# Optimization experiments

Measured on AMD Instinct MI355X. Metric: run time of the kernel, lower is better.

The kernel has to match this reference:

```python
import math
import jax, jax.numpy as jnp
import numpy as np

V, D, H, L, F, S, B = 32000, 768, 12, 6, 3072, 2048, 4
DK = D // H


def setup_inputs() -> dict:
    key = jax.random.key(0)
    ks = jax.random.split(key, 16)
    sc = 0.02
    n = jax.random.normal
    inp = {
        "input_ids": jax.random.randint(ks[0], (B, S), 0, V, dtype=jnp.int64)
        if jax.config.jax_enable_x64 else jax.random.randint(ks[0], (B, S), 0, V, dtype=jnp.int32),
        "emb": n(ks[1], (V, D), jnp.float32) * sc,
        "Wq": n(ks[2], (L, D, D), jnp.float32) * sc, "bq": jnp.zeros((L, D), jnp.float32),
        "Wk": n(ks[3], (L, D, D), jnp.float32) * sc, "bk": jnp.zeros((L, D), jnp.float32),
        "Wv": n(ks[4], (L, D, D), jnp.float32) * sc, "bv": jnp.zeros((L, D), jnp.float32),
        "Wo": n(ks[5], (L, D, D), jnp.float32) * sc, "bo": jnp.zeros((L, D), jnp.float32),
        "W1": n(ks[6], (L, D, F), jnp.float32) * sc, "b1": jnp.zeros((L, F), jnp.float32),
        "W2": n(ks[7], (L, F, D), jnp.float32) * sc, "b2": jnp.zeros((L, D), jnp.float32),
        "gamma": jnp.ones((L, D), jnp.float32), "beta": jnp.zeros((L, D), jnp.float32),
    }
    return inp


def _pos_encoding(seq_len, d):
    pos = jnp.arange(seq_len, dtype=jnp.float32)[:, None]                  # [S,1]
    div = jnp.exp(jnp.arange(0, d, 2, dtype=jnp.float32) * (-math.log(10000.0) / d))
    ang = pos * div                                                        # [S,D/2]
    return jnp.stack([jnp.sin(ang), jnp.cos(ang)], axis=-1).reshape(seq_len, d)


def _layernorm(x, g, b, eps=1e-5):
    mu = x.mean(-1, keepdims=True)
    var = ((x - mu) ** 2).mean(-1, keepdims=True)
    return (x - mu) * jax.lax.rsqrt(var + eps) * g + b


def _forward(input_ids, emb, Wq, bq, Wk, bk, Wv, bv, Wo, bo, W1, b1, W2, b2, gamma, beta):
    mask = (input_ids != 1)[:, None, None, :]                              # [B,1,1,S]
    x = emb[input_ids] + _pos_encoding(input_ids.shape[1], emb.shape[1])   # [B,S,D]

    def layer(x, p):
        wq, bq_, wk, bk_, wv, bv_, wo, bo_, w1, b1_, w2, b2_, g, bt = p
        def heads(h):  # [B,S,D] -> [B,H,S,DK]
            return h.reshape(B, S, H, DK).transpose(0, 2, 1, 3)
        q = heads(x @ wq + bq_)
        k = heads(x @ wk + bk_)
        v = heads(x @ wv + bv_)
        scores = jnp.einsum("bhqd,bhkd->bhqk", q, k) / math.sqrt(DK)
        scores = jnp.where(mask, scores, -1e9)
        attn = jax.nn.softmax(scores, axis=-1)
        o = jnp.einsum("bhqk,bhkd->bhqd", attn, v)
        o = o.transpose(0, 2, 1, 3).reshape(B, S, D) @ wo + bo_
        x1 = _layernorm(x + o, g, bt)
        ff = jax.nn.relu(x1 @ w1 + b1_) @ w2 + b2_
        return _layernorm(x1 + ff, g, bt), None  # same norm params reused (as in source)

    x, _ = jax.lax.scan(layer, x, (Wq, bq, Wk, bk, Wv, bv, Wo, bo, W1, b1, W2, b2, gamma, beta))
    return x.mean(axis=1)                                                  # [B,D]


def reference(input_ids, emb, Wq, bq, Wk, bk, Wv, bv, Wo, bo, W1, b1, W2, b2, gamma, beta):
    return _forward(input_ids, emb, Wq, bq, Wk, bk, Wv, bv, Wo, bo, W1, b1, W2, b2, gamma, beta)
```

## Files before the change

kernel.cpp:

```cpp
#include <hip/hip_runtime.h>
#include <hip/hip_bf16.h>
#include <math.h>

typedef unsigned short u16;
typedef unsigned long long u64;
using bf16x8 = __attribute__((ext_vector_type(8))) short;
using f32x4  = __attribute__((ext_vector_type(4))) float;

static constexpr int kD = 768;
static constexpr int kH = 12;
static constexpr int kL = 6;
static constexpr int kF = 3072;
static constexpr int kS = 2048;
static constexpr int kB = 4;
static constexpr int kQW = 2304;
static constexpr int kNT = kB * kS;

static constexpr float kQScale = 0.18033688011112043f;

__device__ __forceinline__ u16 f2bf(float f) {
    return __bfloat16_as_ushort(__float2bfloat16(f));
}
__device__ __forceinline__ float b2f(u16 u) {
    return __uint_as_float((unsigned)u << 16);
}
__device__ __forceinline__ unsigned cvtpk(float a, float b) {
    unsigned d;
    asm volatile("v_cvt_pk_bf16_f32 %0, %1, %2" : "=v"(d) : "v"(a), "v"(b));
    return d;
}
__device__ __forceinline__ float exp2fast(float x) {
#if __has_builtin(__builtin_amdgcn_exp2f)
    return __builtin_amdgcn_exp2f(x);
#else
    return __expf(x * 0.6931471805599453f);
#endif
}

__device__ __forceinline__ void gload16(const void* g, void* l) {
    auto gp = reinterpret_cast<const __attribute__((address_space(1))) unsigned int*>(
        reinterpret_cast<uintptr_t>(g));
    auto lp = reinterpret_cast<__attribute__((address_space(3))) unsigned int*>(
        reinterpret_cast<uintptr_t>(l));
    __builtin_amdgcn_global_load_lds(gp, lp, 16, 0, 0);
}

__global__ __launch_bounds__(256) void embed_pe(
    const int* __restrict__ ids, const float* __restrict__ emb,
    u16* __restrict__ xbf)
{
    const int t = blockIdx.x;
    const int s = t & (kS - 1);
    const int id = ids[t];
#pragma unroll
    for (int j = 0; j < 3; ++j) {
        const int d = threadIdx.x + (j << 8);
        const float i2 = (float)((d >> 1) << 1);
        const float dv = __expf(i2 * (-9.210340371976184f / 768.f));
        const float ang = (float)s * dv;
        const float pe = (d & 1) ? cosf(ang) : sinf(ang);
        xbf[(size_t)t * kD + d] = f2bf(emb[(size_t)id * kD + d] + pe);
    }
}

__global__ __launch_bounds__(256) void embed_pe_f32(
    const int* __restrict__ ids, const float* __restrict__ emb,
    float* __restrict__ x)
{
    const int t = blockIdx.x;
    const int s = t & (kS - 1);
    const int id = ids[t];
#pragma unroll
    for (int j = 0; j < 3; ++j) {
        const int d = threadIdx.x + (j << 8);
        const float i2 = (float)((d >> 1) << 1);
        const float dv = __expf(i2 * (-9.210340371976184f / 768.f));
        const float ang = (float)s * dv;
        const float pe = (d & 1) ? cosf(ang) : sinf(ang);
        x[(size_t)t * kD + d] = emb[(size_t)id * kD + d] + pe;
    }
}

__global__ __launch_bounds__(64) void mk_maskbits(const int* __restrict__ ids,
                                                  u64* __restrict__ mbits)
{
    const int w = blockIdx.x;
    const int lane = threadIdx.x;
    const u64 m = __ballot(ids[(size_t)w * 64 + lane] != 1);
    if (lane == 0) mbits[w] = m;
}

__global__ __launch_bounds__(256) void bias_build(
    const float* __restrict__ bq, const float* __restrict__ bk,
    const float* __restrict__ bv, const float* __restrict__ bo,
    const float* __restrict__ b1, const float* __restrict__ b2,
    float* __restrict__ ba)
{
    const int i = blockIdx.x * 256 + threadIdx.x;
    if (i >= 6 * 6912) return;
    const int l = i / 6912, p = i % 6912;
    float v;
    if      (p < 768)  v = bq[l * 768 + p] * kQScale;
    else if (p < 1536) v = bk[l * 768 + p - 768];
    else if (p < 2304) v = bv[l * 768 + p - 1536];
    else if (p < 3072) v = bo[l * 768 + p - 2304];
    else if (p < 6144) v = b1[(size_t)l * 3072 + p - 3072];
    else               v = b2[l * 768 + p - 6144];
    ba[i] = v;
}

static constexpr size_t OFF_WO = (size_t)2304 * 768;
static constexpr size_t OFF_W1 = OFF_WO + (size_t)768 * 768;
static constexpr size_t OFF_W2 = OFF_W1 + (size_t)3072 * 768;
static constexpr size_t WARENA_E = OFF_W2 + (size_t)768 * 3072;

__global__ __launch_bounds__(256) void cvt_all(
    const float* __restrict__ Wq, const float* __restrict__ Wk,
    const float* __restrict__ Wv, const float* __restrict__ Wo,
    const float* __restrict__ W1, const float* __restrict__ W2,
    u16* __restrict__ wa)
{
    __shared__ float T[64][68];
    const int t = blockIdx.x;
    const float* S; u16* Dp; int Nsrc, Kdst, srow0, scol0; float sc = 1.f;
    if (t < 432) {
        const int ni = t % 36, ki = t / 36;
        const int ng = ni * 64;
        const int sel = ng / 768;
        scol0 = ng % 768; srow0 = ki * 64;
        S = (sel == 0) ? Wq : (sel == 1) ? Wk : Wv;
        if (sel == 0) sc = kQScale;
        Nsrc = 768; Kdst = 768;
        Dp = wa + (size_t)ng * 768 + srow0;
    } else if (t < 576) {
        const int tt = t - 432; const int ni = tt % 12, ki = tt / 12;
        scol0 = ni * 64; srow0 = ki * 64;
        S = Wo; Nsrc = 768; Kdst = 768;
        Dp = wa + OFF_WO + (size_t)(ni * 64) * 768 + srow0;
    } else if (t < 1152) {
        const int tt = t - 576; const int ni = tt % 48, ki = tt / 48;
        scol0 = ni * 64; srow0 = ki * 64;
        S = W1; Nsrc = 3072; Kdst = 768;
        Dp = wa + OFF_W1 + (size_t)(ni * 64) * 768 + srow0;
    } else {
        const int tt = t - 1152; const int ni = tt % 12, ki = tt / 12;
        scol0 = ni * 64; srow0 = ki * 64;
        S = W2; Nsrc = 768; Kdst = 3072;
        Dp = wa + OFF_W2 + (size_t)(ni * 64) * 3072 + srow0;
    }
    const int tid = threadIdx.x;
#pragma unroll
    for (int i = 0; i < 4; ++i) {
        const int idx = tid + (i << 8);
        const int kr = idx >> 4;
        const int nc = (idx & 15) << 2;
        const float4 v = *(const float4*)(S + (size_t)(srow0 + kr) * Nsrc + scol0 + nc);
        T[kr][nc] = v.x; T[kr][nc + 1] = v.y; T[kr][nc + 2] = v.z; T[kr][nc + 3] = v.w;
    }
    __syncthreads();
#pragma unroll
    for (int i = 0; i < 4; ++i) {
        const int idx = tid + (i << 8);
        const int nr = idx >> 4;
        const int kc = (idx & 15) << 2;
        ushort4 o;
        o.x = f2bf(T[kc][nr] * sc);     o.y = f2bf(T[kc + 1][nr] * sc);
        o.z = f2bf(T[kc + 2][nr] * sc); o.w = f2bf(T[kc + 3][nr] * sc);
        *(ushort4*)(Dp + (size_t)nr * Kdst + kc) = o;
    }
}

__global__ __launch_bounds__(256, 2) void gemm256b(
    const u16* __restrict__ A, const u16* __restrict__ Bt,
    const float* __restrict__ bias, void* __restrict__ Cv,
    u16* __restrict__ vTp, int M, int N, int K, int mode)
{
    __shared__ u16 As[3][4096];
    __shared__ u16 Bs[3][8192];
    const int tid = threadIdx.x;
    const int l = tid & 63;
    const int lo = l & 15, hi = l >> 4;
    const int wc = tid >> 6;

    int brow = blockIdx.x, bcol = blockIdx.y;
    const int gx = gridDim.x;
    if ((gx & 7) == 0) {
        const int id = blockIdx.y * gx + blockIdx.x;
        const int xcd = id & 7, idx = id >> 3;
        const int rpx = gx >> 3;
        brow = xcd * rpx + (idx % rpx);
        bcol = idx / rpx;
    }
    const size_t row0 = (size_t)brow * 128;
    const size_t col0 = (size_t)bcol * 256;

    const int ca0 = tid, ca1 = tid + 256;
    const int ra0 = ca0 >> 2, ga0 = (ca0 & 3) ^ ((ra0 >> 1) & 3);
    const int ra1 = ca1 >> 2, ga1 = (ca1 & 3) ^ ((ra1 >> 1) & 3);
    const u16* aP0 = A + (row0 + ra0) * K + ga0 * 8;
    const u16* aP1 = A + (row0 + ra1) * K + ga1 * 8;
    const u16* bP[4];
#pragma unroll
    for (int q = 0; q < 4; ++q) {
        const int c = tid + (q << 8);
        const int r = c >> 2, g = (c & 3) ^ ((r >> 1) & 3);
        bP[q] = Bt + (col0 + r) * K + g * 8;
    }

    f32x4 acc[8][4];
#pragma unroll
    for (int i = 0; i < 8; ++i)
#pragma unroll
        for (int j = 0; j < 4; ++j)
#pragma unroll
            for (int r = 0; r < 4; ++r) acc[i][j][r] = 0.f;

    int aoff[8], boff[4];
#pragma unroll
    for (int i = 0; i < 8; ++i) {
        const int ra = i * 16 + lo;
        aoff[i] = ra * 32 + ((hi ^ ((ra >> 1) & 3)) << 3);
    }
#pragma unroll
    for (int j = 0; j < 4; ++j) {
        const int rb = wc * 64 + j * 16 + lo;
        boff[j] = rb * 32 + ((hi ^ ((rb >> 1) & 3)) << 3);
    }

    const int NT = K >> 5;
#pragma unroll
    for (int t = 0; t < 2; ++t) {
        const int k0 = t << 5;
        gload16(aP0 + k0, As[t] + ca0 * 8);
        gload16(aP1 + k0, As[t] + ca1 * 8);
#pragma unroll
        for (int q = 0; q < 4; ++q)
            gload16(bP[q] + k0, Bs[t] + (tid + (q << 8)) * 8);
    }

    int cur = 0;
    for (int t = 0; t < NT; ++t) {
        if (t + 1 < NT) {
            asm volatile("s_waitcnt vmcnt(6)" ::: "memory");
        } else {
            asm volatile("s_waitcnt vmcnt(0)" ::: "memory");
        }
        __builtin_amdgcn_s_barrier();
        if (t + 2 < NT) {
            const int k0 = (t + 2) << 5;
            const int nb = (cur + 2 >= 3) ? cur - 1 : cur + 2;
            gload16(aP0 + k0, As[nb] + ca0 * 8);
            gload16(aP1 + k0, As[nb] + ca1 * 8);
#pragma unroll
            for (int q = 0; q < 4; ++q)
                gload16(bP[q] + k0, Bs[nb] + (tid + (q << 8)) * 8);
        }
        bf16x8 af[8], bfr[4];
#pragma unroll
        for (int i = 0; i < 8; ++i) af[i]  = *(const bf16x8*)&As[cur][aoff[i]];
#pragma unroll
        for (int j = 0; j < 4; ++j) bfr[j] = *(const bf16x8*)&Bs[cur][boff[j]];
        __builtin_amdgcn_s_setprio(1);
#pragma unroll
        for (int i = 0; i < 8; ++i)
#pragma unroll
            for (int j = 0; j < 4; ++j)
                acc[i][j] = __builtin_amdgcn_mfma_f32_16x16x32_bf16(
                    af[i], bfr[j], acc[i][j], 0, 0, 0);
        __builtin_amdgcn_s_setprio(0);
        cur = (cur + 1 == 3) ? 0 : cur + 1;
    }

    const bool vmode = (mode == 3) && (col0 >= 1536);
    if (vmode) {
#pragma unroll
        for (int i = 0; i < 8; ++i) {
            const size_t rbase = row0 + i * 16 + hi * 4;
            const size_t tb = (rbase >> 6) * 64;
            const int k0 = (int)(rbase & 63);
            const int pos = (((k0 >> 2) & 3) << 3) + (((k0 >> 4) & 1) << 2)
                          + ((k0 >> 5) << 5);
#pragma unroll
            for (int j = 0; j < 4; ++j) {
                const size_t c = col0 + wc * 64 + j * 16 + lo;
                const float bs = bias[c];
                const size_t d = c - 1536;
                ushort4 o;
                o.x = f2bf(acc[i][j][0] + bs);
                o.y = f2bf(acc[i][j][1] + bs);
                o.z = f2bf(acc[i][j][2] + bs);
                o.w = f2bf(acc[i][j][3] + bs);
                *(ushort4*)(vTp + d * (size_t)M + tb + pos) = o;
            }
        }
        return;
    }

#pragma unroll
    for (int i = 0; i < 8; ++i) {
        const size_t rbase = row0 + i * 16 + hi * 4;
#pragma unroll
        for (int j = 0; j < 4; ++j) {
            const size_t c = col0 + wc * 64 + j * 16 + lo;
            const float bs = bias[c];
#pragma unroll
            for (int r = 0; r < 4; ++r) {
                float v = acc[i][j][r] + bs;
                if (mode == 2) v = fmaxf(v, 0.f);
                ((u16*)Cv)[(rbase + r) * (size_t)N + c] = f2bf(v);
            }
        }
    }
}

__global__ __launch_bounds__(256) void gemm_bf16(
    const u16* __restrict__ A, const u16* __restrict__ Bt,
    const float* __restrict__ bias, void* __restrict__ Cv,
    u16* __restrict__ vTp, int M, int N, int K, int mode)
{
    __shared__ u16 As[3][4096];
    __shared__ u16 Bs[3][4096];
    const int tid = threadIdx.x;
    const int l = tid & 63;
    const int lo = l & 15, hi = l >> 4;
    const int w = tid >> 6, wr = w >> 1, wc = w & 1;

    int brow = blockIdx.x, bcol = blockIdx.y;
    const int gx = gridDim.x;
    if ((gx & 7) == 0) {
        const int id = blockIdx.y * gx + blockIdx.x;
        const int xcd = id & 7, idx = id >> 3;
        const int rpx = gx >> 3;
        brow = xcd * rpx + (idx % rpx);
        bcol = idx / rpx;
    }
    const size_t row0 = (size_t)brow * 128;
    const size_t col0 = (size_t)bcol * 128;

    const int c0 = tid, c1 = tid + 256;
    const int r0 = c0 >> 2, g0 = (c0 & 3) ^ ((r0 >> 1) & 3);
    const int r1 = c1 >> 2, g1 = (c1 & 3) ^ ((r1 >> 1) & 3);
    const u16* a0 = A  + (row0 + r0) * K + g0 * 8;
    const u16* a1 = A  + (row0 + r1) * K + g1 * 8;
    const u16* b0 = Bt + (col0 + r0) * K + g0 * 8;
    const u16* b1 = Bt + (col0 + r1) * K + g1 * 8;

    f32x4 acc[4][4];
#pragma unroll
    for (int i = 0; i < 4; ++i)
#pragma unroll
        for (int j = 0; j < 4; ++j)
#pragma unroll
            for (int r = 0; r < 4; ++r) acc[i][j][r] = 0.f;

    int aoff[4], boff[4];
#pragma unroll
    for (int i = 0; i < 4; ++i) {
        const int ra = wr * 64 + i * 16 + lo;
        aoff[i] = ra * 32 + ((hi ^ ((ra >> 1) & 3)) << 3);
        const int rb = wc * 64 + i * 16 + lo;
        boff[i] = rb * 32 + ((hi ^ ((rb >> 1) & 3)) << 3);
    }

    const int NT = K >> 5;
#pragma unroll
    for (int t = 0; t < 2; ++t) {
        const int k0 = t << 5;
        gload16(a0 + k0, As[t] + c0 * 8);
        gload16(a1 + k0, As[t] + c1 * 8);
        gload16(b0 + k0, Bs[t] + c0 * 8);
        gload16(b1 + k0, Bs[t] + c1 * 8);
    }

    int cur = 0;
    for (int t = 0; t < NT; ++t) {
        if (t + 1 < NT) {
            asm volatile("s_waitcnt vmcnt(4)" ::: "memory");
        } else {
            asm volatile("s_waitcnt vmcnt(0)" ::: "memory");
        }
        __builtin_amdgcn_s_barrier();
        if (t + 2 < NT) {
            const int k0 = (t + 2) << 5;
            const int nb = (cur + 2 >= 3) ? cur - 1 : cur + 2;
            gload16(a0 + k0, As[nb] + c0 * 8);
            gload16(a1 + k0, As[nb] + c1 * 8);
            gload16(b0 + k0, Bs[nb] + c0 * 8);
            gload16(b1 + k0, Bs[nb] + c1 * 8);
        }
        bf16x8 af[4], bfr[4];
#pragma unroll
        for (int i = 0; i < 4; ++i) af[i]  = *(const bf16x8*)&As[cur][aoff[i]];
#pragma unroll
        for (int j = 0; j < 4; ++j) bfr[j] = *(const bf16x8*)&Bs[cur][boff[j]];
        __builtin_amdgcn_s_setprio(1);
#pragma unroll
        for (int i = 0; i < 4; ++i)
#pragma unroll
            for (int j = 0; j < 4; ++j)
                acc[i][j] = __builtin_amdgcn_mfma_f32_16x16x32_bf16(
                    af[i], bfr[j], acc[i][j], 0, 0, 0);
        __builtin_amdgcn_s_setprio(0);
        cur = (cur + 1 == 3) ? 0 : cur + 1;
    }

#pragma unroll
    for (int i = 0; i < 4; ++i) {
        const size_t rbase = row0 + wr * 64 + i * 16 + hi * 4;
#pragma unroll
        for (int j = 0; j < 4; ++j) {
            const size_t c = col0 + wc * 64 + j * 16 + lo;
            const float bs = bias[c];
#pragma unroll
            for (int r = 0; r < 4; ++r) {
                float v = acc[i][j][r] + bs;
                if (mode == 2) v = fmaxf(v, 0.f);
                ((u16*)Cv)[(rbase + r) * (size_t)N + c] = f2bf(v);
            }
        }
    }
}

__global__ __launch_bounds__(512) void attn_mfma(
    const u16* __restrict__ QKV, const u16* __restrict__ vT,
    const u64* __restrict__ mbits, u16* __restrict__ O)
{
    __shared__ u16 Ks[3][4096];
    __shared__ u16 Vs[3][4096];

    const int tid = threadIdx.x, l = tid & 63, w = tid >> 6;
    const int lo = l & 15, hi = l >> 4;

    const int flat = blockIdx.x + 16 * (blockIdx.y + 12 * blockIdx.z);
    const int nf = (flat & 7) * 96 + (flat >> 3);
    const int qi = nf & 15;
    const int h  = (nf >> 4) % 12;
    const int b  = nf / 192;
    const int q0 = qi << 7;

    bf16x8 qf0, qf1;
    {
        const u16* qp = QKV + ((size_t)(b * kS + q0 + w * 16 + lo)) * kQW
                            + h * 64 + hi * 8;
        qf0 = *(const bf16x8*)qp;
        qf1 = *(const bf16x8*)(qp + 32);
    }

    const int rw = tid >> 3, sx = tid & 7, E = sx ^ (rw & 7);
    const u16* Kbase = QKV + (size_t)(b * kS) * kQW + 768 + h * 64;
    const u16* Vbase = vT + (size_t)(h * 64) * kNT + b * kS;

    f32x4 accO[4];
#pragma unroll
    for (int n = 0; n < 4; ++n)
#pragma unroll
        for (int r = 0; r < 4; ++r) accO[n][r] = 0.f;
    float m = -3.0e38f, lsum = 0.f;

    const int ksw = (lo & 7) << 3;
    constexpr int NTt = kS / 64;

#pragma unroll
    for (int t = 0; t < 2; ++t) {
        const size_t kof = (size_t)(t << 6) * kQW;
        const size_t vof = (size_t)(t << 6);
        gload16(Kbase + kof + (size_t)rw * kQW + E * 8, Ks[t] + tid * 8);
        gload16(Vbase + (size_t)rw * kNT + vof + E * 8, Vs[t] + tid * 8);
    }

    int cur = 0;
    for (int kt = 0; kt < NTt; ++kt) {
        if (kt + 1 < NTt) {
            asm volatile("s_waitcnt vmcnt(2)" ::: "memory");
        } else {
            asm volatile("s_waitcnt vmcnt(0)" ::: "memory");
        }
        __syncthreads();

        if (kt + 2 < NTt) {
            const size_t kof = (size_t)((kt + 2) << 6) * kQW;
            const size_t vof = (size_t)((kt + 2) << 6);
            const int nb = (cur + 2 >= 3) ? cur - 1 : cur + 2;
            gload16(Kbase + kof + (size_t)rw * kQW + E * 8, Ks[nb] + tid * 8);
            gload16(Vbase + (size_t)rw * kNT + vof + E * 8, Vs[nb] + tid * 8);
        }

        f32x4 st[4];
        __builtin_amdgcn_s_setprio(1);
#pragma unroll
        for (int j = 0; j < 4; ++j) {
#pragma unroll
            for (int r = 0; r < 4; ++r) st[j][r] = 0.f;
            const int kb2 = (j * 16 + lo) * 64;
            const bf16x8 k0 = *(const bf16x8*)&Ks[cur][kb2 + ((hi * 8)      ^ ksw)];
            const bf16x8 k1 = *(const bf16x8*)&Ks[cur][kb2 + ((hi * 8 + 32) ^ ksw)];
            st[j] = __builtin_amdgcn_mfma_f32_16x16x32_bf16(k0, qf0, st[j], 0, 0, 0);
            st[j] = __builtin_amdgcn_mfma_f32_16x16x32_bf16(k1, qf1, st[j], 0, 0, 0);
        }
        __builtin_amdgcn_s_setprio(0);

        float rmax = st[0][0];
#pragma unroll
        for (int j = 0; j < 4; ++j)
#pragma unroll
            for (int r = 0; r < 4; ++r) rmax = fmaxf(rmax, st[j][r]);
        rmax = fmaxf(rmax, __shfl_xor(rmax, 16));
        rmax = fmaxf(rmax, __shfl_xor(rmax, 32));

        const bool skip = __all(rmax <= m + 11.0f);
        if (!skip) {
            const float mn = fmaxf(m, rmax);
            const float corr = exp2fast(m - mn);
            m = mn;
            lsum *= corr;
            float c2[4];
#pragma unroll
            for (int r = 0; r < 4; ++r) c2[r] = __shfl(corr, hi * 4 + r);
#pragma unroll
            for (int n = 0; n < 4; ++n)
#pragma unroll
                for (int r = 0; r < 4; ++r) accO[n][r] *= c2[r];
        }

#pragma unroll
        for (int j = 0; j < 4; ++j)
#pragma unroll
            for (int r = 0; r < 4; ++r) st[j][r] = exp2fast(st[j][r] - m);

        const u64 mb = mbits[b * 32 + kt];
        if (mb != ~0ull) {
#pragma unroll
            for (int j = 0; j < 4; ++j)
#pragma unroll
                for (int r = 0; r < 4; ++r)
                    if (!((mb >> (j * 16 + hi * 4 + r)) & 1)) st[j][r] = 0.f;
        }

        float ts = 0.f;
#pragma unroll
        for (int j = 0; j < 4; ++j)
#pragma unroll
            for (int r = 0; r < 4; ++r) ts += st[j][r];
        ts += __shfl_xor(ts, 16);
        ts += __shfl_xor(ts, 32);
        lsum += ts;

        union PU { unsigned u[4]; bf16x8 v; } p0, p1;
        p0.u[0] = cvtpk(st[0][0], st[0][1]); p0.u[1] = cvtpk(st[0][2], st[0][3]);
        p0.u[2] = cvtpk(st[1][0], st[1][1]); p0.u[3] = cvtpk(st[1][2], st[1][3]);
        p1.u[0] = cvtpk(st[2][0], st[2][1]); p1.u[1] = cvtpk(st[2][2], st[2][3]);
        p1.u[2] = cvtpk(st[3][0], st[3][1]); p1.u[3] = cvtpk(st[3][2], st[3][3]);

        __builtin_amdgcn_s_setprio(1);
#pragma unroll
        for (int n = 0; n < 4; ++n) {
            const int vb2 = (n * 16 + lo) * 64;
            const bf16x8 v0 = *(const bf16x8*)&Vs[cur][vb2 + ((hi * 8)      ^ ksw)];
            const bf16x8 v1 = *(const bf16x8*)&Vs[cur][vb2 + ((hi * 8 + 32) ^ ksw)];
            accO[n] = __builtin_amdgcn_mfma_f32_16x16x32_bf16(p0.v, v0, accO[n], 0, 0, 0);
            accO[n] = __builtin_amdgcn_mfma_f32_16x16x32_bf16(p1.v, v1, accO[n], 0, 0, 0);
        }
        __builtin_amdgcn_s_setprio(0);
        cur = (cur + 1 == 3) ? 0 : cur + 1;
    }

    float linv[4];
#pragma unroll
    for (int r = 0; r < 4; ++r) linv[r] = 1.f / __shfl(lsum, hi * 4 + r);
#pragma unroll
    for (int n = 0; n < 4; ++n)
#pragma unroll
        for (int r = 0; r < 4; ++r)
            O[((size_t)(b * kS + q0 + w * 16 + hi * 4 + r)) * kD
              + h * 64 + n * 16 + lo] = f2bf(accO[n][r] * linv[r]);
}

__global__ __launch_bounds__(256) void add_ln_bf(
    const u16* __restrict__ a, const u16* __restrict__ r,
    const float* __restrict__ g, const float* __restrict__ bt,
    u16* __restrict__ out)
{
    const int lane = threadIdx.x & 63;
    const size_t row = (size_t)blockIdx.x * 4 + (threadIdx.x >> 6);
    const ushort4* a4 = (const ushort4*)(a + row * kD);
    const ushort4* r4 = (const ushort4*)(r + row * kD);
    float v[3][4];
    float s = 0.f;
#pragma unroll
    for (int j = 0; j < 3; ++j) {
        const ushort4 av = a4[j * 64 + lane];
        const ushort4 rv = r4[j * 64 + lane];
        v[j][0] = b2f(av.x) + b2f(rv.x);
        v[j][1] = b2f(av.y) + b2f(rv.y);
        v[j][2] = b2f(av.z) + b2f(rv.z);
        v[j][3] = b2f(av.w) + b2f(rv.w);
        s += v[j][0] + v[j][1] + v[j][2] + v[j][3];
    }
#pragma unroll
    for (int off = 32; off; off >>= 1) s += __shfl_xor(s, off);
    const float mu = s * (1.f / 768.f);
    float vs = 0.f;
#pragma unroll
    for (int j = 0; j < 3; ++j)
#pragma unroll
        for (int e = 0; e < 4; ++e) {
            const float t0 = v[j][e] - mu;
            vs = fmaf(t0, t0, vs);
        }
#pragma unroll
    for (int off = 32; off; off >>= 1) vs += __shfl_xor(vs, off);
    const float rstd = rsqrtf(vs * (1.f / 768.f) + 1e-5f);
    const float4* g4 = (const float4*)g;
    const float4* b4 = (const float4*)bt;
#pragma unroll
    for (int j = 0; j < 3; ++j) {
        const float4 gv = g4[j * 64 + lane];
        const float4 bv = b4[j * 64 + lane];
        ushort4 o;
        o.x = f2bf((v[j][0] - mu) * rstd * gv.x + bv.x);
        o.y = f2bf((v[j][1] - mu) * rstd * gv.y + bv.y);
        o.z = f2bf((v[j][2] - mu) * rstd * gv.z + bv.z);
        o.w = f2bf((v[j][3] - mu) * rstd * gv.w + bv.w);
        ((ushort4*)(out + row * kD))[j * 64 + lane] = o;
    }
}

__global__ __launch_bounds__(192) void mean_part_bf(
    const u16* __restrict__ x, float* __restrict__ mred)
{
    const int c = blockIdx.x, b = blockIdx.y;
    const int d = threadIdx.x * 4;
    const u16* base = x + ((size_t)b * kS + c * 32) * kD + d;
    float s0 = 0.f, s1 = 0.f, s2 = 0.f, s3 = 0.f;
#pragma unroll 8
    for (int t = 0; t < 32; ++t) {
        const ushort4 u = *(const ushort4*)(base + (size_t)t * kD);
        s0 += b2f(u.x); s1 += b2f(u.y); s2 += b2f(u.z); s3 += b2f(u.w);
    }
    float4 o; o.x = s0; o.y = s1; o.z = s2; o.w = s3;
    *(float4*)(mred + ((size_t)b * 64 + c) * kD + d) = o;
}

__global__ __launch_bounds__(256) void mean_fin(
    const float* __restrict__ mred, float* __restrict__ out)
{
    const int d = blockIdx.x * 256 + threadIdx.x;
    const int b = blockIdx.y;
    float s = 0.f;
#pragma unroll
    for (int c = 0; c < 64; ++c) s += mred[((size_t)b * 64 + c) * kD + d];
    out[b * kD + d] = s * (1.f / 2048.f);
}

__global__ __launch_bounds__(256) void add_ln_f32(
    const float* __restrict__ a, const float* __restrict__ r,
    const float* __restrict__ g, const float* __restrict__ bt,
    float* __restrict__ out)
{
    const int lane = threadIdx.x & 63;
    const size_t row = (size_t)blockIdx.x * 4 + (threadIdx.x >> 6);
    const float4* a4 = (const float4*)(a + row * kD);
    const float4* r4 = (const float4*)(r + row * kD);
    float4 v[3];
    float s = 0.f;
#pragma unroll
    for (int j = 0; j < 3; ++j) {
        const float4 av = a4[j * 64 + lane];
        const float4 rv = r4[j * 64 + lane];
        v[j].x = av.x + rv.x; v[j].y = av.y + rv.y;
        v[j].z = av.z + rv.z; v[j].w = av.w + rv.w;
        s += v[j].x + v[j].y + v[j].z + v[j].w;
    }
#pragma unroll
    for (int off = 32; off; off >>= 1) s += __shfl_xor(s, off);
    const float mu = s * (1.f / 768.f);
    float vs = 0.f;
#pragma unroll
    for (int j = 0; j < 3; ++j) {
        float t0 = v[j].x - mu, t1 = v[j].y - mu, t2 = v[j].z - mu, t3 = v[j].w - mu;
        vs = fmaf(t0, t0, fmaf(t1, t1, fmaf(t2, t2, fmaf(t3, t3, vs))));
    }
#pragma unroll
    for (int off = 32; off; off >>= 1) vs += __shfl_xor(vs, off);
    const float rstd = rsqrtf(vs * (1.f / 768.f) + 1e-5f);
    const float4* g4 = (const float4*)g;
    const float4* b4 = (const float4*)bt;
#pragma unroll
    for (int j = 0; j < 3; ++j) {
        const float4 gv = g4[j * 64 + lane];
        const float4 bv = b4[j * 64 + lane];
        float4 o;
        o.x = (v[j].x - mu) * rstd * gv.x + bv.x;
        o.y = (v[j].y - mu) * rstd * gv.y + bv.y;
        o.z = (v[j].z - mu) * rstd * gv.z + bv.z;
        o.w = (v[j].w - mu) * rstd * gv.w + bv.w;
        ((float4*)(out + row * kD))[j * 64 + lane] = o;
    }
}

__global__ __launch_bounds__(256) void mean_s(
    const float* __restrict__ x, float* __restrict__ out)
{
    const int d = blockIdx.x * 256 + threadIdx.x;
    const int b = blockIdx.y;
    float s = 0.f;
    for (int t = 0; t < kS; ++t) s += x[((size_t)b * kS + t) * kD + d];
    out[b * kD + d] = s * (1.f / 2048.f);
}

__global__ __launch_bounds__(256) void gemm_f32(
    const float* __restrict__ A, const float* __restrict__ W,
    const float* __restrict__ bias, float* __restrict__ C,
    int M, int N, int K, int relu)
{
    __shared__ float As[16][68];
    __shared__ float Bs[16][68];
    const int tid = threadIdx.x;
    const int row0 = blockIdx.x << 6;
    const int col0 = blockIdx.y << 6;
    const int tx = tid & 15, ty = tid >> 4;
    const int ar = tid >> 2;
    const int ak = (tid & 3) << 2;
    const int bk = tid >> 4;
    const int bc = (tid & 15) << 2;
    float acc[4][4] = {};
    const float* Ap = A + (size_t)(row0 + ar) * K + ak;
    const float* Wp = W + (size_t)bk * N + col0 + bc;
    for (int k0 = 0; k0 < K; k0 += 16) {
        const float4 a4 = *(const float4*)(Ap + k0);
        const float4 b4 = *(const float4*)(Wp + (size_t)k0 * N);
        __syncthreads();
        As[ak + 0][ar] = a4.x; As[ak + 1][ar] = a4.y;
        As[ak + 2][ar] = a4.z; As[ak + 3][ar] = a4.w;
        *(float4*)&Bs[bk][bc] = b4;
        __syncthreads();
#pragma unroll
        for (int kk = 0; kk < 16; ++kk) {
            const float4 av = *(const float4*)&As[kk][ty << 2];
            const float4 bv = *(const float4*)&Bs[kk][tx << 2];
            const float aa[4] = {av.x, av.y, av.z, av.w};
            const float bb[4] = {bv.x, bv.y, bv.z, bv.w};
#pragma unroll
            for (int i = 0; i < 4; ++i)
#pragma unroll
                for (int j = 0; j < 4; ++j)
                    acc[i][j] = fmaf(aa[i], bb[j], acc[i][j]);
        }
    }
#pragma unroll
    for (int i = 0; i < 4; ++i) {
        const int row = row0 + (ty << 2) + i;
#pragma unroll
        for (int j = 0; j < 4; ++j) {
            const int col = col0 + (tx << 2) + j;
            float v = acc[i][j] + bias[col];
            if (relu) v = fmaxf(v, 0.f);
            C[(size_t)row * N + col] = v;
        }
    }
}

__global__ __launch_bounds__(256) void attn_fused(
    const float* __restrict__ Q, const float* __restrict__ Km,
    const float* __restrict__ Vm, const int* __restrict__ ids,
    float* __restrict__ O)
{
    __shared__ float Ksf[64 * 64];
    __shared__ float Vtf[64 * 64];
    __shared__ float Qs[16][64];
    __shared__ float Psf[4][4][64];
    const int tid = threadIdx.x;
    const int w = tid >> 6;
    const int lane = tid & 63;
    const int h = blockIdx.y, b = blockIdx.z;
    const int qrow0 = blockIdx.x << 4;
    {
        const int r = tid >> 4;
        const int c4 = tid & 15;
        const float4 q4 = *(const float4*)(
            Q + ((size_t)(b * kS + qrow0 + r)) * kD + h * 64 + (c4 << 2));
        Qs[r][(c4 << 2) + 0] = q4.x * 0.125f;
        Qs[r][(c4 << 2) + 1] = q4.y * 0.125f;
        Qs[r][(c4 << 2) + 2] = q4.z * 0.125f;
        Qs[r][(c4 << 2) + 3] = q4.w * 0.125f;
    }
    float m[4], lsum[4], o[4];
#pragma unroll
    for (int r = 0; r < 4; ++r) { m[r] = -3.0e38f; lsum[r] = 0.f; o[r] = 0.f; }
    for (int kt = 0; kt < kS / 64; ++kt) {
        __syncthreads();
#pragma unroll
        for (int i = 0; i < 4; ++i) {
            const int lin = tid + (i << 8);
            const int row = lin >> 4;
            const int s4 = lin & 15;
            const size_t gro = ((size_t)(b * kS + (kt << 6) + row)) * kD + h * 64 + (s4 << 2);
            const float4 k4 = *(const float4*)(Km + gro);
            ((float4*)Ksf)[(row << 4) + (s4 ^ (row & 7))] = k4;
            const float4 v4 = *(const float4*)(Vm + gro);
            const int ksl = row >> 2, ke = row & 3;
            const int d0 = s4 << 2;
            Vtf[(d0 + 0) * 64 + ((ksl ^ ((d0 + 0) & 7)) << 2) + ke] = v4.x;
            Vtf[(d0 + 1) * 64 + ((ksl ^ ((d0 + 1) & 7)) << 2) + ke] = v4.y;
            Vtf[(d0 + 2) * 64 + ((ksl ^ ((d0 + 2) & 7)) << 2) + ke] = v4.z;
            Vtf[(d0 + 3) * 64 + ((ksl ^ ((d0 + 3) & 7)) << 2) + ke] = v4.w;
        }
        __syncthreads();
        const bool masked = (ids[(size_t)b * kS + (kt << 6) + lane] == 1);
        float scr[4] = {0.f, 0.f, 0.f, 0.f};
#pragma unroll
        for (int i16 = 0; i16 < 16; ++i16) {
            const float4 kv = ((const float4*)Ksf)[(lane << 4) + (i16 ^ (lane & 7))];
#pragma unroll
            for (int r = 0; r < 4; ++r) {
                const float4 qv = *(const float4*)&Qs[(w << 2) + r][i16 << 2];
                scr[r] = fmaf(kv.x, qv.x, fmaf(kv.y, qv.y,
                          fmaf(kv.z, qv.z, fmaf(kv.w, qv.w, scr[r]))));
            }
        }
#pragma unroll
        for (int r = 0; r < 4; ++r) {
            float sm = masked ? -3.0e38f : scr[r];
#pragma unroll
            for (int off = 32; off; off >>= 1) sm = fmaxf(sm, __shfl_xor(sm, off));
            const float mn = fmaxf(m[r], sm);
            const float cr = __expf(m[r] - mn);
            const float pv = masked ? 0.f : __expf(scr[r] - mn);
            float ps = pv;
#pragma unroll
            for (int off = 32; off; off >>= 1) ps += __shfl_xor(ps, off);
            lsum[r] = lsum[r] * cr + ps;
            o[r] *= cr;
            m[r] = mn;
            Psf[w][r][lane] = pv;
        }
#pragma unroll
        for (int i16 = 0; i16 < 16; ++i16) {
            const float4 vv = ((const float4*)Vtf)[(lane << 4) + (i16 ^ (lane & 7))];
#pragma unroll
            for (int r = 0; r < 4; ++r) {
                const float4 pv = *(const float4*)&Psf[w][r][i16 << 2];
                o[r] = fmaf(pv.x, vv.x, fmaf(pv.y, vv.y,
                        fmaf(pv.z, vv.z, fmaf(pv.w, vv.w, o[r]))));
            }
        }
    }
#pragma unroll
    for (int r = 0; r < 4; ++r)
        O[((size_t)(b * kS + qrow0 + (w << 2) + r)) * kD + h * 64 + lane] =
            o[r] / lsum[r];
}

extern "C" void kernel_launch(void* const* d_in, const int* in_sizes, int n_in,
                              void* d_out, int out_size, void* d_ws, size_t ws_size,
                              hipStream_t stream)
{
    const int*   ids   = (const int*)  d_in[0];
    const float* emb   = (const float*)d_in[1];
    const float* Wq    = (const float*)d_in[2];
    const float* bq    = (const float*)d_in[3];
    const float* Wk    = (const float*)d_in[4];
    const float* bk    = (const float*)d_in[5];
    const float* Wv    = (const float*)d_in[6];
    const float* bv    = (const float*)d_in[7];
    const float* Wo    = (const float*)d_in[8];
    const float* bo    = (const float*)d_in[9];
    const float* W1    = (const float*)d_in[10];
    const float* b1    = (const float*)d_in[11];
    const float* W2    = (const float*)d_in[12];
    const float* b2    = (const float*)d_in[13];
    const float* gamma = (const float*)d_in[14];
    const float* beta  = (const float*)d_in[15];
    float* out = (float*)d_out;

    const size_t BUFE = (size_t)kB * kS * kD;
    const size_t WDD  = (size_t)kD * kD;
    const size_t WDF  = (size_t)kD * kF;
    const size_t HIDE = (size_t)kB * kS * kF;
    const int NTOK = kB * kS;

    const size_t NEED = BUFE * 2 * 4
                      + HIDE * 2
                      + WARENA_E * 2
                      + (size_t)6 * 6912 * 4
                      + 128 * 8
                      + (size_t)kB * 64 * kD * 4;

    if (ws_size >= NEED) {
        u16*   xb  = (u16*)d_ws;
        u16*   x1b = xb + BUFE;
        u16*   ao  = x1b + BUFE;
        u16*   ob  = ao + BUFE;
        u16*   sc  = ob + BUFE;
        u16*   vtb = sc + (size_t)NTOK * kQW;
        u16*   wa  = sc + HIDE;
        float* ba  = (float*)(wa + WARENA_E);
        u64*   mbt = (u64*)(ba + 6 * 6912);
        float* mrd = (float*)(mbt + 128);

        embed_pe<<<NTOK, 256, 0, stream>>>(ids, emb, xb);
        mk_maskbits<<<kB * kS / 64, 64, 0, stream>>>(ids, mbt);
        bias_build<<<(6 * 6912 + 255) / 256, 256, 0, stream>>>(
            bq, bk, bv, bo, b1, b2, ba);

        for (int l = 0; l < kL; ++l) {
            const size_t oDD = (size_t)l * WDD;
            const size_t oDF = (size_t)l * WDF;
            const float* bl = ba + (size_t)l * 6912;
            const float* gl  = gamma + (size_t)l * kD;
            const float* btl = beta  + (size_t)l * kD;

            cvt_all<<<1728, 256, 0, stream>>>(
                Wq + oDD, Wk + oDD, Wv + oDD, Wo + oDD, W1 + oDF, W2 + oDF, wa);

            gemm256b<<<dim3(64, 9), 256, 0, stream>>>(
                xb, wa, bl, sc, vtb, NTOK, kQW, kD, 3);

            attn_mfma<<<dim3(kS / 128, kH, kB), 512, 0, stream>>>(
                sc, vtb, mbt, ao);

            gemm_bf16<<<dim3(64, 6), 256, 0, stream>>>(
                ao, wa + OFF_WO, bl + 2304, ob, nullptr, NTOK, kD, kD, 1);

            add_ln_bf<<<NTOK / 4, 256, 0, stream>>>(xb, ob, gl, btl, x1b);

            gemm256b<<<dim3(64, 12), 256, 0, stream>>>(
                x1b, wa + OFF_W1, bl + 3072, sc, nullptr, NTOK, kF, kD, 2);
            gemm_bf16<<<dim3(64, 6), 256, 0, stream>>>(
                sc, wa + OFF_W2, bl + 6144, ob, nullptr, NTOK, kD, kF, 1);

            add_ln_bf<<<NTOK / 4, 256, 0, stream>>>(x1b, ob, gl, btl, xb);
        }

        mean_part_bf<<<dim3(64, kB), 192, 0, stream>>>(xb, mrd);
        mean_fin<<<dim3(kD / 256, kB), 256, 0, stream>>>(mrd, out);
        return;
    }

    if (ws_size < 5 * BUFE * sizeof(float)) return;
    float* xb = (float*)d_ws;
    float* kb = xb + BUFE;
    float* qb = kb + BUFE;
    float* vb = qb + BUFE;
    float* obf = vb + BUFE;
    float* hb = qb;

    embed_pe_f32<<<NTOK, 256, 0, stream>>>(ids, emb, xb);
    for (int l = 0; l < kL; ++l) {
        const size_t oDD = (size_t)l * WDD;
        const size_t oDF = (size_t)l * WDF;
        gemm_f32<<<dim3(NTOK / 64, kD / 64), 256, 0, stream>>>(
            xb, Wq + oDD, bq + (size_t)l * kD, qb, NTOK, kD, kD, 0);
        gemm_f32<<<dim3(NTOK / 64, kD / 64), 256, 0, stream>>>(
            xb, Wk + oDD, bk + (size_t)l * kD, kb, NTOK, kD, kD, 0);
        gemm_f32<<<dim3(NTOK / 64, kD / 64), 256, 0, stream>>>(
            xb, Wv + oDD, bv + (size_t)l * kD, vb, NTOK, kD, kD, 0);
        attn_fused<<<dim3(kS / 16, kH, kB), 256, 0, stream>>>(qb, kb, vb, ids, obf);
        gemm_f32<<<dim3(NTOK / 64, kD / 64), 256, 0, stream>>>(
            obf, Wo + oDD, bo + (size_t)l * kD, qb, NTOK, kD, kD, 0);
        add_ln_f32<<<NTOK / 4, 256, 0, stream>>>(xb, qb,
            gamma + (size_t)l * kD, beta + (size_t)l * kD, kb);
        for (int c = 0; c < 2; ++c) {
            const size_t ro = (size_t)c * 4096;
            gemm_f32<<<dim3(4096 / 64, kF / 64), 256, 0, stream>>>(
                kb + ro * kD, W1 + oDF, b1 + (size_t)l * kF, hb, 4096, kF, kD, 1);
            gemm_f32<<<dim3(4096 / 64, kD / 64), 256, 0, stream>>>(
                hb, W2 + oDF, b2 + (size_t)l * kD, obf + ro * kD, 4096, kD, kF, 0);
        }
        add_ln_f32<<<NTOK / 4, 256, 0, stream>>>(kb, obf,
            gamma + (size_t)l * kD, beta + (size_t)l * kD, xb);
    }
    mean_s<<<dim3(kD / 256, kB), 256, 0, stream>>>(xb, out);
}
```

Baseline: 1.528 ms.

## Process two key tiles per attention iteration and defer row-sum reduction

The attention kernel now handles 128 keys per loop iteration as two 64-key tiles. It uses four LDS buffers arranged as a double-buffered pair, and issues the next pair's K/V loads once per iteration after a full vmcnt(0) wait. This halves the number of barriers, max reductions and rescale steps per key. The per-lane row sum is now reduced across lanes only once, after the loop. In exchange, LDS use grows from 48KB to 64KB, which may lower occupancy, and prefetch depth shrinks from two tiles ahead to one pair ahead.

Measured after the change: 1.485 ms (median of 2 runs). 1.03x faster.

```diff
diff --git a/kernel.cpp b/kernel.cpp
--- a/kernel.cpp
+++ b/kernel.cpp
@@ -425,8 +425,8 @@
     const u16* __restrict__ QKV, const u16* __restrict__ vT,
     const u64* __restrict__ mbits, u16* __restrict__ O)
 {
-    __shared__ u16 Ks[3][4096];
-    __shared__ u16 Vs[3][4096];
+    __shared__ u16 Ks[4][4096];
+    __shared__ u16 Vs[4][4096];
 
     const int tid = threadIdx.x, l = tid & 63, w = tid >> 6;
     const int lo = l & 15, hi = l >> 4;
@@ -458,7 +458,7 @@
     float m = -3.0e38f, lsum = 0.f;
 
     const int ksw = (lo & 7) << 3;
-    constexpr int NTt = kS / 64;
+    constexpr int NP = kS / 128;
 
 #pragma unroll
     for (int t = 0; t < 2; ++t) {
@@ -468,42 +468,49 @@
         gload16(Vbase + (size_t)rw * kNT + vof + E * 8, Vs[t] + tid * 8);
     }
 
-    int cur = 0;
-    for (int kt = 0; kt < NTt; ++kt) {
-        if (kt + 1 < NTt) {
-            asm volatile("s_waitcnt vmcnt(2)" ::: "memory");
-        } else {
-            asm volatile("s_waitcnt vmcnt(0)" ::: "memory");
-        }
+    for (int it = 0; it < NP; ++it) {
+        const int bA = (it & 1) << 1, bB = bA + 1;
+        asm volatile("s_waitcnt vmcnt(0)" ::: "memory");
         __syncthreads();
 
-        if (kt + 2 < NTt) {
-            const size_t kof = (size_t)((kt + 2) << 6) * kQW;
-            const size_t vof = (size_t)((kt + 2) << 6);
-            const int nb = (cur + 2 >= 3) ? cur - 1 : cur + 2;
-            gload16(Kbase + kof + (size_t)rw * kQW + E * 8, Ks[nb] + tid * 8);
-            gload16(Vbase + (size_t)rw * kNT + vof + E * 8, Vs[nb] + tid * 8);
-        }
-
-        f32x4 st[4];
+        if (it + 1 < NP) {
+            const int nA = ((it + 1) & 1) << 1, nB = nA + 1;
+            const size_t kofA = (size_t)((2 * it + 2) << 6) * kQW;
+            const size_t kofB = (size_t)((2 * it + 3) << 6) * kQW;
+            const size_t vofA = (size_t)((2 * it + 2) << 6);
+            const size_t vofB = (size_t)((2 * it + 3) << 6);
+            gload16(Kbase + kofA + (size_t)rw * kQW + E * 8, Ks[nA] + tid * 8);
+            gload16(Vbase + (size_t)rw * kNT + vofA + E * 8, Vs[nA] + tid * 8);
+            gload16(Kbase + kofB + (size_t)rw * kQW + E * 8, Ks[nB] + tid * 8);
+            gload16(Vbase + (size_t)rw * kNT + vofB + E * 8, Vs[nB] + tid * 8);
+        }
+
+        f32x4 stA[4], stB[4];
         __builtin_amdgcn_s_setprio(1);
 #pragma unroll
         for (int j = 0; j < 4; ++j) {
 #pragma unroll
-            for (int r = 0; r < 4; ++r) st[j][r] = 0.f;
+            for (int r = 0; r < 4; ++r) { stA[j][r] = 0.f; stB[j][r] = 0.f; }
             const int kb2 = (j * 16 + lo) * 64;
-            const bf16x8 k0 = *(const bf16x8*)&Ks[cur][kb2 + ((hi * 8)      ^ ksw)];
-            const bf16x8 k1 = *(const bf16x8*)&Ks[cur][kb2 + ((hi * 8 + 32) ^ ksw)];
-            st[j] = __builtin_amdgcn_mfma_f32_16x16x32_bf16(k0, qf0, st[j], 0, 0, 0);
-            st[j] = __builtin_amdgcn_mfma_f32_16x16x32_bf16(k1, qf1, st[j], 0, 0, 0);
+            const bf16x8 a0 = *(const bf16x8*)&Ks[bA][kb2 + ((hi * 8)      ^ ksw)];
+            const bf16x8 a1 = *(const bf16x8*)&Ks[bA][kb2 + ((hi * 8 + 32) ^ ksw)];
+            const bf16x8 b0v = *(const bf16x8*)&Ks[bB][kb2 + ((hi * 8)      ^ ksw)];
+            const bf16x8 b1v = *(const bf16x8*)&Ks[bB][kb2 + ((hi * 8 + 32) ^ ksw)];
+            stA[j] = __builtin_amdgcn_mfma_f32_16x16x32_bf16(a0, qf0, stA[j], 0, 0, 0);
+            stA[j] = __builtin_amdgcn_mfma_f32_16x16x32_bf16(a1, qf1, stA[j], 0, 0, 0);
+            stB[j] = __builtin_amdgcn_mfma_f32_16x16x32_bf16(b0v, qf0, stB[j], 0, 0, 0);
+            stB[j] = __builtin_amdgcn_mfma_f32_16x16x32_bf16(b1v, qf1, stB[j], 0, 0, 0);
         }
         __builtin_amdgcn_s_setprio(0);
 
-        float rmax = st[0][0];
+        float rmax = stA[0][0];
 #pragma unroll
         for (int j = 0; j < 4; ++j)
 #pragma unroll
-            for (int r = 0; r < 4; ++r) rmax = fmaxf(rmax, st[j][r]);
+            for (int r = 0; r < 4; ++r) {
+                rmax = fmaxf(rmax, stA[j][r]);
+                rmax = fmaxf(rmax, stB[j][r]);
+            }
         rmax = fmaxf(rmax, __shfl_xor(rmax, 16));
         rmax = fmaxf(rmax, __shfl_xor(rmax, 32));
 
@@ -525,48 +532,67 @@
 #pragma unroll
         for (int j = 0; j < 4; ++j)
 #pragma unroll
-            for (int r = 0; r < 4; ++r) st[j][r] = exp2fast(st[j][r] - m);
-
-        const u64 mb = mbits[b * 32 + kt];
-        if (mb != ~0ull) {
+            for (int r = 0; r < 4; ++r) {
+                stA[j][r] = exp2fast(stA[j][r] - m);
+                stB[j][r] = exp2fast(stB[j][r] - m);
+            }
+
+        const u64 mbA = mbits[b * 32 + 2 * it];
+        const u64 mbB = mbits[b * 32 + 2 * it + 1];
+        if (mbA != ~0ull) {
 #pragma unroll
             for (int j = 0; j < 4; ++j)
 #pragma unroll
                 for (int r = 0; r < 4; ++r)
-                    if (!((mb >> (j * 16 + hi * 4 + r)) & 1)) st[j][r] = 0.f;
+                    if (!((mbA >> (j * 16 + hi * 4 + r)) & 1)) stA[j][r] = 0.f;
+        }
+        if (mbB != ~0ull) {
+#pragma unroll
+            for (int j = 0; j < 4; ++j)
+#pragma unroll
+                for (int r = 0; r < 4; ++r)
+                    if (!((mbB >> (j * 16 + hi * 4 + r)) & 1)) stB[j][r] = 0.f;
         }
 
         float ts = 0.f;
 #pragma unroll
         for (int j = 0; j < 4; ++j)
 #pragma unroll
-            for (int r = 0; r < 4; ++r) ts += st[j][r];
-        ts += __shfl_xor(ts, 16);
-        ts += __shfl_xor(ts, 32);
+            for (int r = 0; r < 4; ++r) ts += stA[j][r] + stB[j][r];
         lsum += ts;
 
-        union PU { unsigned u[4]; bf16x8 v; } p0, p1;
-        p0.u[0] = cvtpk(st[0][0], st[0][1]); p0.u[1] = cvtpk(st[0][2], st[0][3]);
-        p0.u[2] = cvtpk(st[1][0], st[1][1]); p0.u[3] = cvtpk(st[1][2], st[1][3]);
-        p1.u[0] = cvtpk(st[2][0], st[2][1]); p1.u[1] = cvtpk(st[2][2], st[2][3]);
-        p1.u[2] = cvtpk(st[3][0], st[3][1]); p1.u[3] = cvtpk(st[3][2], st[3][3]);
+        union PU { unsigned u[4]; bf16x8 v; } p0, p1, p2, p3;
+        p0.u[0] = cvtpk(stA[0][0], stA[0][1]); p0.u[1] = cvtpk(stA[0][2], stA[0][3]);
+        p0.u[2] = cvtpk(stA[1][0], stA[1][1]); p0.u[3] = cvtpk(stA[1][2], stA[1][3]);
+        p1.u[0] = cvtpk(stA[2][0], stA[2][1]); p1.u[1] = cvtpk(stA[2][2], stA[2][3]);
+        p1.u[2] = cvtpk(stA[3][0], stA[3][1]); p1.u[3] = cvtpk(stA[3][2], stA[3][3]);
+        p2.u[0] = cvtpk(stB[0][0], stB[0][1]); p2.u[1] = cvtpk(stB[0][2], stB[0][3]);
+        p2.u[2] = cvtpk(stB[1][0], stB[1][1]); p2.u[3] = cvtpk(stB[1][2], stB[1][3]);
+        p3.u[0] = cvtpk(stB[2][0], stB[2][1]); p3.u[1] = cvtpk(stB[2][2], stB[2][3]);
+        p3.u[2] = cvtpk(stB[3][0], stB[3][1]); p3.u[3] = cvtpk(stB[3][2], stB[3][3]);
 
         __builtin_amdgcn_s_setprio(1);
 #pragma unroll
         for (int n = 0; n < 4; ++n) {
             const int vb2 = (n * 16 + lo) * 64;
-            const bf16x8 v0 = *(const bf16x8*)&Vs[cur][vb2 + ((hi * 8)      ^ ksw)];
-            const bf16x8 v1 = *(const bf16x8*)&Vs[cur][vb2 + ((hi * 8 + 32) ^ ksw)];
-            accO[n] = __builtin_amdgcn_mfma_f32_16x16x32_bf16(p0.v, v0, accO[n], 0, 0, 0);
-            accO[n] = __builtin_amdgcn_mfma_f32_16x16x32_bf16(p1.v, v1, accO[n], 0, 0, 0);
+            const bf16x8 vA0 = *(const bf16x8*)&Vs[bA][vb2 + ((hi * 8)      ^ ksw)];
+            const bf16x8 vA1 = *(const bf16x8*)&Vs[bA][vb2 + ((hi * 8 + 32) ^ ksw)];
+            const bf16x8 vB0 = *(const bf16x8*)&Vs[bB][vb2 + ((hi * 8)      ^ ksw)];
+            const bf16x8 vB1 = *(const bf16x8*)&Vs[bB][vb2 + ((hi * 8 + 32) ^ ksw)];
+            accO[n] = __builtin_amdgcn_mfma_f32_16x16x32_bf16(p0.v, vA0, accO[n], 0, 0, 0);
+            accO[n] = __builtin_amdgcn_mfma_f32_16x16x32_bf16(p1.v, vA1, accO[n], 0, 0, 0);
+            accO[n] = __builtin_amdgcn_mfma_f32_16x16x32_bf16(p2.v, vB0, accO[n], 0, 0, 0);
+            accO[n] = __builtin_amdgcn_mfma_f32_16x16x32_bf16(p3.v, vB1, accO[n], 0, 0, 0);
         }
         __builtin_amdgcn_s_setprio(0);
-        cur = (cur + 1 == 3) ? 0 : cur + 1;
-    }
-
+    }
+
+    float ts = lsum;
+    ts += __shfl_xor(ts, 16);
+    ts += __shfl_xor(ts, 32);
     float linv[4];
 #pragma unroll
-    for (int r = 0; r < 4; ++r) linv[r] = 1.f / __shfl(lsum, hi * 4 + r);
+    for (int r = 0; r < 4; ++r) linv[r] = 1.f / __shfl(ts, hi * 4 + r);
 #pragma unroll
     for (int n = 0; n < 4; ++n)
 #pragma unroll
```
